# Kernel optimization log

Measured on AMD Instinct MI355X. Metric: run time of the kernel, lower is better.

Reference implementation:

```python
import jax, jax.numpy as jnp
import numpy as np

N, D, DFF, E, TOPK = 32768, 256, 1024, 8, 2


def setup_inputs() -> dict:
    key = jax.random.key(0)
    ks = jax.random.split(key, 5)
    return {
        "x": jax.random.normal(ks[0], (N, D), dtype=jnp.float32),
        "gate_w": jax.random.normal(ks[1], (D, E), dtype=jnp.float32) * 0.02,
        "gate_b": jnp.zeros((E,), jnp.float32),
        "w1": jax.random.normal(ks[2], (E, D, DFF), dtype=jnp.float32) * 0.02,
        "b1": jnp.zeros((E, DFF), jnp.float32),
        "w2": jax.random.normal(ks[3], (E, DFF, D), dtype=jnp.float32) * 0.02,
        "b2": jnp.zeros((E, D), jnp.float32),
        "top_k": TOPK,
    }


def reference(x, gate_w, gate_b, w1, b1, w2, b2, top_k):
    # Gating network: linear -> softmax -> top-k (returns topk_vals, topk_idx)
    logits = x @ gate_w + gate_b                       # [N, E]
    probs = jax.nn.softmax(logits, axis=-1)
    topk_vals, topk_idx = jax.lax.top_k(probs, top_k)  # [N, K], [N, K]

    # Naive full-batch expert evaluation (every expert runs on every token),
    # faithful to the original loop that applies the selected expert to all of x.
    h = jax.nn.relu(jnp.einsum('nd,edf->enf', x, w1) + b1[:, None, :])  # [E, N, DFF]
    y = jnp.einsum('enf,efd->end', h, w2) + b2[:, None, :]              # [E, N, D]

    # Per-token gather of the top-k experts' outputs, then weighted sum.
    y = jnp.transpose(y, (1, 0, 2))                                      # [N, E, D]
    sel = jnp.take_along_axis(y, topk_idx[:, :, None], axis=1)           # [N, K, D]
    return jnp.sum(sel * topk_vals[:, :, None], axis=1)                  # [N, D]
```

## Files before the change

### kernel.cpp

```cpp
#include <hip/hip_runtime.h>

#define N_TOK 32768
#define D 256
#define DFF 1024
#define NE 8
#define TB 64

typedef __attribute__((ext_vector_type(16))) float f32x16;
typedef __attribute__((ext_vector_type(8)))  short bf16x8;

#define BARRIER() do {                                        \
    asm volatile("s_waitcnt lgkmcnt(0)" ::: "memory");        \
    __builtin_amdgcn_s_barrier();                             \
    __builtin_amdgcn_sched_barrier(0);                        \
} while (0)

__device__ __forceinline__ unsigned short f2bf(float f) {
    union { float f; unsigned u; } v; v.f = f;
    unsigned r = v.u + 0x7FFFu + ((v.u >> 16) & 1u);
    return (unsigned short)(r >> 16);
}

__global__ __launch_bounds__(256) void wf_prep(
    const float* __restrict__ w1, const float* __restrict__ w2,
    short* __restrict__ w1f, short* __restrict__ w2f) {
    const int b = blockIdx.x;
    if (b < 1024) {
        const int gid  = b * 256 + threadIdx.x;
        const int lane = gid & 63;
        const int frag = gid >> 6;
        const int dblk = frag & 15;
        const int fblk = (frag >> 4) & 31;
        const int e    = frag >> 9;
        const int l31 = lane & 31, g = lane >> 5;

        const float* src = w1 + ((size_t)e * 256 + dblk * 16 + g * 8) * 1024
                              + fblk * 32 + l31;
        unsigned u[4];
#pragma unroll
        for (int jp = 0; jp < 4; ++jp) {
            float a = src[(size_t)(jp * 2)     * 1024];
            float c = src[(size_t)(jp * 2 + 1) * 1024];
            u[jp] = (unsigned)f2bf(a) | ((unsigned)f2bf(c) << 16);
        }
        *(uint4*)(w1f + (size_t)gid * 8) = make_uint4(u[0], u[1], u[2], u[3]);
    } else {
        const int gid  = (b - 1024) * 256 + threadIdx.x;
        const int lane = gid & 63;
        const int frag = gid >> 6;
        const int fblk = frag & 63;
        const int cblk = (frag >> 6) & 7;
        const int e    = frag >> 9;
        const int l31 = lane & 31, g = lane >> 5;

        const float* src = w2 + ((size_t)e * 1024 + fblk * 16 + g * 8) * 256
                              + cblk * 32 + l31;
        unsigned u[4];
#pragma unroll
        for (int jp = 0; jp < 4; ++jp) {
            float a = src[(size_t)(jp * 2)     * 256];
            float c = src[(size_t)(jp * 2 + 1) * 256];
            u[jp] = (unsigned)f2bf(a) | ((unsigned)f2bf(c) << 16);
        }
        *(uint4*)(w2f + (size_t)gid * 8) = make_uint4(u[0], u[1], u[2], u[3]);
    }
}

__global__ __launch_bounds__(256) void gate_all(
    const float* __restrict__ x, const float* __restrict__ gw,
    const float* __restrict__ gb,
    int* __restrict__ cnt, int* __restrict__ bidx, float* __restrict__ bp,
    int2* __restrict__ opos) {
    __shared__ float gws[2048];
    __shared__ int   se1[256], se2[256];
    __shared__ float sp1[256], sp2[256];
    __shared__ int   hist[NE], base_[NE];

    const int tid = threadIdx.x;
#pragma unroll
    for (int i = 0; i < 8; ++i) gws[tid + 256 * i] = gw[tid + 256 * i];
    if (tid < NE) hist[tid] = 0;
    __syncthreads();

    const int t = blockIdx.x * 256 + tid;
    const float* xr = x + (size_t)t * D;

    double acc[NE];
#pragma unroll
    for (int e = 0; e < NE; ++e) acc[e] = 0.0;

    for (int d0 = 0; d0 < 256; d0 += 4) {
        float4 xv = *(const float4*)(xr + d0);
        float xa[4] = {xv.x, xv.y, xv.z, xv.w};
#pragma unroll
        for (int j = 0; j < 4; ++j) {
            float4 ga  = *(const float4*)&gws[(d0 + j) * 8];
            float4 gbb = *(const float4*)&gws[(d0 + j) * 8 + 4];
            double xd = (double)xa[j];
            acc[0] += xd * (double)ga.x;  acc[1] += xd * (double)ga.y;
            acc[2] += xd * (double)ga.z;  acc[3] += xd * (double)ga.w;
            acc[4] += xd * (double)gbb.x; acc[5] += xd * (double)gbb.y;
            acc[6] += xd * (double)gbb.z; acc[7] += xd * (double)gbb.w;
        }
    }

    double l[NE];
#pragma unroll
    for (int e = 0; e < NE; ++e) l[e] = acc[e] + (double)gb[e];
    int e1 = 0;
#pragma unroll
    for (int e = 1; e < NE; ++e) if (l[e] > l[e1]) e1 = e;
    int e2 = (e1 == 0) ? 1 : 0;
#pragma unroll
    for (int e = 0; e < NE; ++e) if (e != e1 && l[e] > l[e2]) e2 = e;

    double s = 0.0;
#pragma unroll
    for (int e = 0; e < NE; ++e) s += exp(l[e] - l[e1]);
    se1[tid] = e1; se2[tid] = e2;
    sp1[tid] = (float)(1.0 / s);
    sp2[tid] = (float)(exp(l[e2] - l[e1]) / s);
    __syncthreads();

    const int pos1 = atomicAdd(&hist[se1[tid]], 1);
    const int pos2 = atomicAdd(&hist[se2[tid]], 1);
    __syncthreads();
    if (tid < NE) base_[tid] = atomicAdd(&cnt[tid], hist[tid]);
    __syncthreads();

    const int o1 = se1[tid] * N_TOK + base_[se1[tid]] + pos1;
    const int o2 = se2[tid] * N_TOK + base_[se2[tid]] + pos2;
    bidx[o1] = t;  bp[o1] = sp1[tid];
    bidx[o2] = t;  bp[o2] = sp2[tid];
    opos[t] = make_int2(o1, o2);
}

__global__ __launch_bounds__(512, 4) void expert_ffn(
    const float* __restrict__ x,
    const short* __restrict__ w1f,
    const short* __restrict__ w2f,
    const float* __restrict__ b1, const float* __restrict__ b2,
    const int* __restrict__ cnt, const int* __restrict__ bidx,
    const float* __restrict__ bp, float* __restrict__ out,
    float* __restrict__ yp, int staged) {
    const int e    = blockIdx.x & 7;
    const int tile = blockIdx.x >> 3;
    const int n_e  = cnt[e];
    const int row0 = tile * TB;
    if (row0 >= n_e) return;

    __shared__ short xs[16 * 64 * 16];
    __shared__ short hs[32 * 512];
    __shared__ int   tok_s[TB];
    __shared__ float p_s[TB];

    const int tid  = threadIdx.x;
    const int lane = tid & 63, wid = tid >> 6;
    const int l31  = lane & 31, g = lane >> 5;

    if (tid < TB) {
        int r = row0 + tid;
        tok_s[tid] = (r < n_e) ? bidx[e * N_TOK + r] : -1;
        p_s[tid]   = (r < n_e) ? bp[e * N_TOK + r] : 0.f;
    }
    BARRIER();

    {
        const int tok = tid >> 3;
        const int tk  = tok_s[tok];
        const float* xrow = x + (size_t)(tk < 0 ? 0 : tk) * D;
#pragma unroll
        for (int i = 0; i < 2; ++i) {
            const int dblk = (tid & 7) * 2 + i;
            unsigned u[8];
            if (tk >= 0) {
#pragma unroll
                for (int q = 0; q < 4; ++q) {
                    float4 v = *(const float4*)(xrow + dblk * 16 + q * 4);
                    u[q * 2 + 0] = (unsigned)f2bf(v.x) | ((unsigned)f2bf(v.y) << 16);
                    u[q * 2 + 1] = (unsigned)f2bf(v.z) | ((unsigned)f2bf(v.w) << 16);
                }
            } else {
#pragma unroll
                for (int q = 0; q < 8; ++q) u[q] = 0;
            }
            short* dp = &xs[dblk * 1024 + tok * 16];
            *(uint4*)(dp)     = make_uint4(u[0], u[1], u[2], u[3]);
            *(uint4*)(dp + 8) = make_uint4(u[4], u[5], u[6], u[7]);
        }
    }

    f32x16 acc[2];
#pragma unroll
    for (int a = 0; a < 2; ++a)
#pragma unroll
        for (int r = 0; r < 16; ++r) acc[a][r] = 0.f;

    const short* w1e = w1f + (size_t)e * (32 * 16 * 512);
    const short* w2e = w2f + (size_t)e * (8 * 64 * 512);
    const float* b1e = b1 + e * DFF;

    BARRIER();

    for (int fc = 0; fc < 4; ++fc) {
        f32x16 h0, h1;
#pragma unroll
        for (int r = 0; r < 16; ++r) { h0[r] = 0.f; h1[r] = 0.f; }

        const short* w1p = w1e + ((size_t)(fc * 8 + wid) * 16) * 512 + lane * 8;
        __builtin_amdgcn_s_setprio(1);
        {
            bf16x8 a0 = *(const bf16x8*)(w1p);
            bf16x8 x0 = *(const bf16x8*)&xs[l31 * 16 + g * 8];
            bf16x8 x1 = *(const bf16x8*)&xs[512 + l31 * 16 + g * 8];
#pragma unroll
            for (int db = 0; db < 16; ++db) {
                bf16x8 an, y0, y1;
                if (db < 15) {
                    an = *(const bf16x8*)(w1p + (db + 1) * 512);
                    y0 = *(const bf16x8*)&xs[(db + 1) * 1024 + l31 * 16 + g * 8];
                    y1 = *(const bf16x8*)&xs[(db + 1) * 1024 + 512 + l31 * 16 + g * 8];
                }
                h0 = __builtin_amdgcn_mfma_f32_32x32x16_bf16(a0, x0, h0, 0, 0, 0);
                h1 = __builtin_amdgcn_mfma_f32_32x32x16_bf16(a0, x1, h1, 0, 0, 0);
                if (db < 15) { a0 = an; x0 = y0; x1 = y1; }
            }
        }
        __builtin_amdgcn_s_setprio(0);

        BARRIER();

#pragma unroll
        for (int tp = 0; tp < 2; ++tp) {
            const f32x16& hh = tp ? h1 : h0;
#pragma unroll
            for (int m = 0; m < 4; ++m) {
                float4 bq = *(const float4*)(b1e + fc * 256 + wid * 32 + 8 * m + 4 * g);
                float v0 = fmaxf(hh[4 * m + 0] + bq.x, 0.f);
                float v1 = fmaxf(hh[4 * m + 1] + bq.y, 0.f);
                float v2 = fmaxf(hh[4 * m + 2] + bq.z, 0.f);
                float v3 = fmaxf(hh[4 * m + 3] + bq.w, 0.f);
                uint2 pk;
                pk.x = (unsigned)f2bf(v0) | ((unsigned)f2bf(v1) << 16);
                pk.y = (unsigned)f2bf(v2) | ((unsigned)f2bf(v3) << 16);
                const int fragid = (2 * wid + (m >> 1)) * 2 + tp;
                *(uint2*)&hs[fragid * 512 + ((m & 1) * 32 + l31) * 8 + 4 * g] = pk;
            }
        }

        const short* w2p = w2e + ((size_t)wid * 64 + fc * 16) * 512 + lane * 8;
        bf16x8 wcur = *(const bf16x8*)(w2p);

        BARRIER();

        __builtin_amdgcn_s_setprio(1);
        {
            bf16x8 ha0 = *(const bf16x8*)&hs[0 * 512 + lane * 8];
            bf16x8 ha1 = *(const bf16x8*)&hs[1 * 512 + lane * 8];
#pragma unroll
            for (int kt = 0; kt < 16; ++kt) {
                bf16x8 wn, hb0, hb1;
                if (kt < 15) {
                    wn  = *(const bf16x8*)(w2p + (kt + 1) * 512);
                    hb0 = *(const bf16x8*)&hs[((kt + 1) * 2 + 0) * 512 + lane * 8];
                    hb1 = *(const bf16x8*)&hs[((kt + 1) * 2 + 1) * 512 + lane * 8];
                }
                acc[0] = __builtin_amdgcn_mfma_f32_32x32x16_bf16(ha0, wcur, acc[0], 0, 0, 0);
                acc[1] = __builtin_amdgcn_mfma_f32_32x32x16_bf16(ha1, wcur, acc[1], 0, 0, 0);
                if (kt < 15) { wcur = wn; ha0 = hb0; ha1 = hb1; }
            }
        }
        __builtin_amdgcn_s_setprio(0);
    }

    const float* b2e = b2 + e * D;
    const int col = wid * 32 + l31;
    const float bv = b2e[col];
    if (staged) {
        float* ype = yp + ((size_t)e * N_TOK + row0) * 256;
#pragma unroll
        for (int tp = 0; tp < 2; ++tp) {
#pragma unroll
            for (int r = 0; r < 16; ++r) {
                const int tl = tp * 32 + (r & 3) + 8 * (r >> 2) + 4 * g;
                if (tok_s[tl] >= 0)
                    __builtin_nontemporal_store(
                        (acc[tp][r] + bv) * p_s[tl],
                        &ype[(size_t)tl * 256 + col]);
            }
        }
    } else {
#pragma unroll
        for (int tp = 0; tp < 2; ++tp) {
#pragma unroll
            for (int r = 0; r < 16; ++r) {
                const int tl = tp * 32 + (r & 3) + 8 * (r >> 2) + 4 * g;
                const int tk = tok_s[tl];
                if (tk >= 0)
                    atomicAdd(out + (size_t)tk * D + col,
                              (acc[tp][r] + bv) * p_s[tl]);
            }
        }
    }
}

__global__ __launch_bounds__(256) void combine(
    const float* __restrict__ yp, const int2* __restrict__ opos,
    float* __restrict__ out) {
    const int gid   = blockIdx.x * 256 + threadIdx.x;
    const int t     = gid >> 6;
    const int lane4 = gid & 63;
    const int2 o = opos[t];
    const float4 a = ((const float4*)yp)[(size_t)o.x * 64 + lane4];
    const float4 b = ((const float4*)yp)[(size_t)o.y * 64 + lane4];
    float4 r;
    r.x = a.x + b.x; r.y = a.y + b.y; r.z = a.z + b.z; r.w = a.w + b.w;
    ((float4*)out)[gid] = r;
}

extern "C" void kernel_launch(void* const* d_in, const int* in_sizes, int n_in,
                              void* d_out, int out_size, void* d_ws, size_t ws_size,
                              hipStream_t stream) {
    const float* x  = (const float*)d_in[0];
    const float* gw = (const float*)d_in[1];
    const float* gb = (const float*)d_in[2];
    const float* w1 = (const float*)d_in[3];
    const float* b1 = (const float*)d_in[4];
    const float* w2 = (const float*)d_in[5];
    const float* b2 = (const float*)d_in[6];
    float* out = (float*)d_out;

    char* ws = (char*)d_ws;
    size_t off = 0;
    int*   cnt   = (int*)(ws + off);  off += 256;
    int*   bidx  = (int*)(ws + off);  off += (size_t)NE * N_TOK * 4;
    float* bp    = (float*)(ws + off); off += (size_t)NE * N_TOK * 4;
    int2*  opos  = (int2*)(ws + off); off += (size_t)N_TOK * 8;
    short* w1f   = (short*)(ws + off); off += (size_t)NE * D * DFF * 2;
    short* w2f   = (short*)(ws + off); off += (size_t)NE * D * DFF * 2;
    float* yp    = (float*)(ws + off); off += (size_t)2 * N_TOK * D * 4;
    const int staged = (ws_size >= off) ? 1 : 0;

    hipMemsetAsync(cnt, 0, 256, stream);
    if (!staged)
        hipMemsetAsync(d_out, 0, (size_t)out_size * sizeof(float), stream);

    wf_prep<<<2048, 256, 0, stream>>>(w1, w2, w1f, w2f);
    gate_all<<<N_TOK / 256, 256, 0, stream>>>(x, gw, gb, cnt, bidx, bp, opos);
    expert_ffn<<<NE * (N_TOK / TB), 512, 0, stream>>>(x, w1f, w2f, b1, b2,
                                                      cnt, bidx, bp, out, yp, staged);
    if (staged)
        combine<<<(N_TOK * D / 4) / 256, 256, 0, stream>>>(yp, opos, out);
}
```

Measured before the change: 159.9 us.

## Merge weight prep with gating and deepen expert weight prefetch

```diff
diff --git a/kernel.cpp b/kernel.cpp
--- a/kernel.cpp
+++ b/kernel.cpp
@@ -21,56 +21,57 @@
     return (unsigned short)(r >> 16);
 }
 
-__global__ __launch_bounds__(256) void wf_prep(
+__global__ __launch_bounds__(256) void prep_gate(
     const float* __restrict__ w1, const float* __restrict__ w2,
-    short* __restrict__ w1f, short* __restrict__ w2f) {
-    const int b = blockIdx.x;
-    if (b < 1024) {
-        const int gid  = b * 256 + threadIdx.x;
-        const int lane = gid & 63;
-        const int frag = gid >> 6;
-        const int dblk = frag & 15;
-        const int fblk = (frag >> 4) & 31;
-        const int e    = frag >> 9;
-        const int l31 = lane & 31, g = lane >> 5;
-
-        const float* src = w1 + ((size_t)e * 256 + dblk * 16 + g * 8) * 1024
-                              + fblk * 32 + l31;
-        unsigned u[4];
-#pragma unroll
-        for (int jp = 0; jp < 4; ++jp) {
-            float a = src[(size_t)(jp * 2)     * 1024];
-            float c = src[(size_t)(jp * 2 + 1) * 1024];
-            u[jp] = (unsigned)f2bf(a) | ((unsigned)f2bf(c) << 16);
-        }
-        *(uint4*)(w1f + (size_t)gid * 8) = make_uint4(u[0], u[1], u[2], u[3]);
-    } else {
-        const int gid  = (b - 1024) * 256 + threadIdx.x;
-        const int lane = gid & 63;
-        const int frag = gid >> 6;
-        const int fblk = frag & 63;
-        const int cblk = (frag >> 6) & 7;
-        const int e    = frag >> 9;
-        const int l31 = lane & 31, g = lane >> 5;
-
-        const float* src = w2 + ((size_t)e * 1024 + fblk * 16 + g * 8) * 256
-                              + cblk * 32 + l31;
-        unsigned u[4];
-#pragma unroll
-        for (int jp = 0; jp < 4; ++jp) {
-            float a = src[(size_t)(jp * 2)     * 256];
-            float c = src[(size_t)(jp * 2 + 1) * 256];
-            u[jp] = (unsigned)f2bf(a) | ((unsigned)f2bf(c) << 16);
-        }
-        *(uint4*)(w2f + (size_t)gid * 8) = make_uint4(u[0], u[1], u[2], u[3]);
-    }
-}
-
-__global__ __launch_bounds__(256) void gate_all(
+    short* __restrict__ w1f, short* __restrict__ w2f,
     const float* __restrict__ x, const float* __restrict__ gw,
     const float* __restrict__ gb,
     int* __restrict__ cnt, int* __restrict__ bidx, float* __restrict__ bp,
     int2* __restrict__ opos) {
+    const int b = blockIdx.x;
+    if (b < 2048) {
+        if (b < 1024) {
+            const int gid  = b * 256 + threadIdx.x;
+            const int lane = gid & 63;
+            const int frag = gid >> 6;
+            const int dblk = frag & 15;
+            const int fblk = (frag >> 4) & 31;
+            const int e    = frag >> 9;
+            const int l31 = lane & 31, g = lane >> 5;
+
+            const float* src = w1 + ((size_t)e * 256 + dblk * 16 + g * 8) * 1024
+                                  + fblk * 32 + l31;
+            unsigned u[4];
+#pragma unroll
+            for (int jp = 0; jp < 4; ++jp) {
+                float a = src[(size_t)(jp * 2)     * 1024];
+                float c = src[(size_t)(jp * 2 + 1) * 1024];
+                u[jp] = (unsigned)f2bf(a) | ((unsigned)f2bf(c) << 16);
+            }
+            *(uint4*)(w1f + (size_t)gid * 8) = make_uint4(u[0], u[1], u[2], u[3]);
+        } else {
+            const int gid  = (b - 1024) * 256 + threadIdx.x;
+            const int lane = gid & 63;
+            const int frag = gid >> 6;
+            const int fblk = frag & 63;
+            const int cblk = (frag >> 6) & 7;
+            const int e    = frag >> 9;
+            const int l31 = lane & 31, g = lane >> 5;
+
+            const float* src = w2 + ((size_t)e * 1024 + fblk * 16 + g * 8) * 256
+                                  + cblk * 32 + l31;
+            unsigned u[4];
+#pragma unroll
+            for (int jp = 0; jp < 4; ++jp) {
+                float a = src[(size_t)(jp * 2)     * 256];
+                float c = src[(size_t)(jp * 2 + 1) * 256];
+                u[jp] = (unsigned)f2bf(a) | ((unsigned)f2bf(c) << 16);
+            }
+            *(uint4*)(w2f + (size_t)gid * 8) = make_uint4(u[0], u[1], u[2], u[3]);
+        }
+        return;
+    }
+
     __shared__ float gws[2048];
     __shared__ int   se1[256], se2[256];
     __shared__ float sp1[256], sp2[256];
@@ -82,7 +83,7 @@
     if (tid < NE) hist[tid] = 0;
     __syncthreads();
 
-    const int t = blockIdx.x * 256 + tid;
+    const int t = (b - 2048) * 256 + tid;
     const float* xr = x + (size_t)t * D;
 
     double acc[NE];
@@ -200,33 +201,47 @@
     const short* w2e = w2f + (size_t)e * (8 * 64 * 512);
     const float* b1e = b1 + e * DFF;
 
+    bf16x8 w1r[4];
+    {
+        const short* w1p0 = w1e + ((size_t)(0 * 8 + wid) * 16) * 512 + lane * 8;
+#pragma unroll
+        for (int k = 0; k < 4; ++k) w1r[k] = *(const bf16x8*)(w1p0 + k * 512);
+    }
+
     BARRIER();
 
     for (int fc = 0; fc < 4; ++fc) {
+        const short* w1p = w1e + ((size_t)(fc * 8 + wid) * 16) * 512 + lane * 8;
+
         f32x16 h0, h1;
 #pragma unroll
         for (int r = 0; r < 16; ++r) { h0[r] = 0.f; h1[r] = 0.f; }
 
-        const short* w1p = w1e + ((size_t)(fc * 8 + wid) * 16) * 512 + lane * 8;
         __builtin_amdgcn_s_setprio(1);
         {
-            bf16x8 a0 = *(const bf16x8*)(w1p);
             bf16x8 x0 = *(const bf16x8*)&xs[l31 * 16 + g * 8];
             bf16x8 x1 = *(const bf16x8*)&xs[512 + l31 * 16 + g * 8];
 #pragma unroll
             for (int db = 0; db < 16; ++db) {
-                bf16x8 an, y0, y1;
+                bf16x8 wa = w1r[db & 3];
+                if (db < 12)
+                    w1r[db & 3] = *(const bf16x8*)(w1p + (db + 4) * 512);
+                bf16x8 y0, y1;
                 if (db < 15) {
-                    an = *(const bf16x8*)(w1p + (db + 1) * 512);
                     y0 = *(const bf16x8*)&xs[(db + 1) * 1024 + l31 * 16 + g * 8];
                     y1 = *(const bf16x8*)&xs[(db + 1) * 1024 + 512 + l31 * 16 + g * 8];
                 }
-                h0 = __builtin_amdgcn_mfma_f32_32x32x16_bf16(a0, x0, h0, 0, 0, 0);
-                h1 = __builtin_amdgcn_mfma_f32_32x32x16_bf16(a0, x1, h1, 0, 0, 0);
-                if (db < 15) { a0 = an; x0 = y0; x1 = y1; }
+                h0 = __builtin_amdgcn_mfma_f32_32x32x16_bf16(wa, x0, h0, 0, 0, 0);
+                h1 = __builtin_amdgcn_mfma_f32_32x32x16_bf16(wa, x1, h1, 0, 0, 0);
+                if (db < 15) { x0 = y0; x1 = y1; }
             }
         }
         __builtin_amdgcn_s_setprio(0);
+
+        const short* w2p = w2e + ((size_t)wid * 64 + fc * 16) * 512 + lane * 8;
+        bf16x8 w2r[4];
+#pragma unroll
+        for (int k = 0; k < 4; ++k) w2r[k] = *(const bf16x8*)(w2p + k * 512);
 
         BARRIER();
 
@@ -248,10 +263,13 @@
             }
         }
 
-        const short* w2p = w2e + ((size_t)wid * 64 + fc * 16) * 512 + lane * 8;
-        bf16x8 wcur = *(const bf16x8*)(w2p);
-
         BARRIER();
+
+        if (fc < 3) {
+            const short* w1n = w1e + ((size_t)((fc + 1) * 8 + wid) * 16) * 512 + lane * 8;
+#pragma unroll
+            for (int k = 0; k < 4; ++k) w1r[k] = *(const bf16x8*)(w1n + k * 512);
+        }
 
         __builtin_amdgcn_s_setprio(1);
         {
@@ -259,15 +277,17 @@
             bf16x8 ha1 = *(const bf16x8*)&hs[1 * 512 + lane * 8];
 #pragma unroll
             for (int kt = 0; kt < 16; ++kt) {
-                bf16x8 wn, hb0, hb1;
+                bf16x8 wa = w2r[kt & 3];
+                if (kt < 12)
+                    w2r[kt & 3] = *(const bf16x8*)(w2p + (kt + 4) * 512);
+                bf16x8 hb0, hb1;
                 if (kt < 15) {
-                    wn  = *(const bf16x8*)(w2p + (kt + 1) * 512);
                     hb0 = *(const bf16x8*)&hs[((kt + 1) * 2 + 0) * 512 + lane * 8];
                     hb1 = *(const bf16x8*)&hs[((kt + 1) * 2 + 1) * 512 + lane * 8];
                 }
-                acc[0] = __builtin_amdgcn_mfma_f32_32x32x16_bf16(ha0, wcur, acc[0], 0, 0, 0);
-                acc[1] = __builtin_amdgcn_mfma_f32_32x32x16_bf16(ha1, wcur, acc[1], 0, 0, 0);
-                if (kt < 15) { wcur = wn; ha0 = hb0; ha1 = hb1; }
+                acc[0] = __builtin_amdgcn_mfma_f32_32x32x16_bf16(ha0, wa, acc[0], 0, 0, 0);
+                acc[1] = __builtin_amdgcn_mfma_f32_32x32x16_bf16(ha1, wa, acc[1], 0, 0, 0);
+                if (kt < 15) { ha0 = hb0; ha1 = hb1; }
             }
         }
         __builtin_amdgcn_s_setprio(0);
@@ -345,8 +365,8 @@
     if (!staged)
         hipMemsetAsync(d_out, 0, (size_t)out_size * sizeof(float), stream);
 
-    wf_prep<<<2048, 256, 0, stream>>>(w1, w2, w1f, w2f);
-    gate_all<<<N_TOK / 256, 256, 0, stream>>>(x, gw, gb, cnt, bidx, bp, opos);
+    prep_gate<<<2048 + N_TOK / 256, 256, 0, stream>>>(
+        w1, w2, w1f, w2f, x, gw, gb, cnt, bidx, bp, opos);
     expert_ffn<<<NE * (N_TOK / TB), 512, 0, stream>>>(x, w1f, w2f, b1, b2,
                                                       cnt, bidx, bp, out, yp, staged);
     if (staged)
```

New measurement: 162.0 us. Within noise of the previous version (+1.3%).

## Fuse weight prep, x bf16 conversion and gating into one kernel; compact staging buffer

Applied to the files above, without the earlier changes.

```diff
diff --git a/kernel.cpp b/kernel.cpp
--- a/kernel.cpp
+++ b/kernel.cpp
@@ -15,15 +15,19 @@
     __builtin_amdgcn_sched_barrier(0);                        \
 } while (0)
 
-__device__ __forceinline__ unsigned short f2bf(float f) {
-    union { float f; unsigned u; } v; v.f = f;
-    unsigned r = v.u + 0x7FFFu + ((v.u >> 16) & 1u);
-    return (unsigned short)(r >> 16);
-}
-
-__global__ __launch_bounds__(256) void wf_prep(
+__device__ __forceinline__ unsigned cvtpk(float lo, float hi) {
+    unsigned r;
+    asm("v_cvt_pk_bf16_f32 %0, %1, %2" : "=v"(r) : "v"(lo), "v"(hi));
+    return r;
+}
+
+__global__ __launch_bounds__(256) void prep_gate(
     const float* __restrict__ w1, const float* __restrict__ w2,
-    short* __restrict__ w1f, short* __restrict__ w2f) {
+    short* __restrict__ w1f, short* __restrict__ w2f,
+    const float* __restrict__ x, short* __restrict__ xb,
+    const float* __restrict__ gw, const float* __restrict__ gb,
+    int* __restrict__ cnt, int* __restrict__ bidx, float* __restrict__ bp,
+    int2* __restrict__ opos) {
     const int b = blockIdx.x;
     if (b < 1024) {
         const int gid  = b * 256 + threadIdx.x;
@@ -38,13 +42,13 @@
                               + fblk * 32 + l31;
         unsigned u[4];
 #pragma unroll
-        for (int jp = 0; jp < 4; ++jp) {
-            float a = src[(size_t)(jp * 2)     * 1024];
-            float c = src[(size_t)(jp * 2 + 1) * 1024];
-            u[jp] = (unsigned)f2bf(a) | ((unsigned)f2bf(c) << 16);
-        }
+        for (int jp = 0; jp < 4; ++jp)
+            u[jp] = cvtpk(src[(size_t)(jp * 2) * 1024],
+                          src[(size_t)(jp * 2 + 1) * 1024]);
         *(uint4*)(w1f + (size_t)gid * 8) = make_uint4(u[0], u[1], u[2], u[3]);
-    } else {
+        return;
+    }
+    if (b < 2048) {
         const int gid  = (b - 1024) * 256 + threadIdx.x;
         const int lane = gid & 63;
         const int frag = gid >> 6;
@@ -57,20 +61,24 @@
                               + cblk * 32 + l31;
         unsigned u[4];
 #pragma unroll
-        for (int jp = 0; jp < 4; ++jp) {
-            float a = src[(size_t)(jp * 2)     * 256];
-            float c = src[(size_t)(jp * 2 + 1) * 256];
-            u[jp] = (unsigned)f2bf(a) | ((unsigned)f2bf(c) << 16);
-        }
+        for (int jp = 0; jp < 4; ++jp)
+            u[jp] = cvtpk(src[(size_t)(jp * 2) * 256],
+                          src[(size_t)(jp * 2 + 1) * 256]);
         *(uint4*)(w2f + (size_t)gid * 8) = make_uint4(u[0], u[1], u[2], u[3]);
-    }
-}
-
-__global__ __launch_bounds__(256) void gate_all(
-    const float* __restrict__ x, const float* __restrict__ gw,
-    const float* __restrict__ gb,
-    int* __restrict__ cnt, int* __restrict__ bidx, float* __restrict__ bp,
-    int2* __restrict__ opos) {
+        return;
+    }
+    if (b < 6144) {
+        const int gid = (b - 2048) * 256 + threadIdx.x;
+        const float* s = x + (size_t)gid * 8;
+        float4 a = *(const float4*)(s);
+        float4 c = *(const float4*)(s + 4);
+        uint4 o;
+        o.x = cvtpk(a.x, a.y);  o.y = cvtpk(a.z, a.w);
+        o.z = cvtpk(c.x, c.y);  o.w = cvtpk(c.z, c.w);
+        *(uint4*)(xb + (size_t)gid * 8) = o;
+        return;
+    }
+
     __shared__ float gws[2048];
     __shared__ int   se1[256], se2[256];
     __shared__ float sp1[256], sp2[256];
@@ -82,7 +90,7 @@
     if (tid < NE) hist[tid] = 0;
     __syncthreads();
 
-    const int t = blockIdx.x * 256 + tid;
+    const int t = (b - 6144) * 256 + tid;
     const float* xr = x + (size_t)t * D;
 
     double acc[NE];
@@ -136,7 +144,7 @@
 }
 
 __global__ __launch_bounds__(512, 4) void expert_ffn(
-    const float* __restrict__ x,
+    const short* __restrict__ xb,
     const short* __restrict__ w1f,
     const short* __restrict__ w2f,
     const float* __restrict__ b1, const float* __restrict__ b2,
@@ -158,6 +166,9 @@
     const int lane = tid & 63, wid = tid >> 6;
     const int l31  = lane & 31, g = lane >> 5;
 
+    int cbase = 0;
+    for (int j = 0; j < e; ++j) cbase += cnt[j];
+
     if (tid < TB) {
         int r = row0 + tid;
         tok_s[tid] = (r < n_e) ? bidx[e * N_TOK + r] : -1;
@@ -168,25 +179,18 @@
     {
         const int tok = tid >> 3;
         const int tk  = tok_s[tok];
-        const float* xrow = x + (size_t)(tk < 0 ? 0 : tk) * D;
+        const short* xrow = xb + (size_t)(tk < 0 ? 0 : tk) * D;
 #pragma unroll
         for (int i = 0; i < 2; ++i) {
             const int dblk = (tid & 7) * 2 + i;
-            unsigned u[8];
+            uint4 v0 = make_uint4(0, 0, 0, 0), v1 = make_uint4(0, 0, 0, 0);
             if (tk >= 0) {
-#pragma unroll
-                for (int q = 0; q < 4; ++q) {
-                    float4 v = *(const float4*)(xrow + dblk * 16 + q * 4);
-                    u[q * 2 + 0] = (unsigned)f2bf(v.x) | ((unsigned)f2bf(v.y) << 16);
-                    u[q * 2 + 1] = (unsigned)f2bf(v.z) | ((unsigned)f2bf(v.w) << 16);
-                }
-            } else {
-#pragma unroll
-                for (int q = 0; q < 8; ++q) u[q] = 0;
+                v0 = *(const uint4*)(xrow + dblk * 16);
+                v1 = *(const uint4*)(xrow + dblk * 16 + 8);
             }
             short* dp = &xs[dblk * 1024 + tok * 16];
-            *(uint4*)(dp)     = make_uint4(u[0], u[1], u[2], u[3]);
-            *(uint4*)(dp + 8) = make_uint4(u[4], u[5], u[6], u[7]);
+            *(uint4*)(dp)     = v0;
+            *(uint4*)(dp + 8) = v1;
         }
     }
 
@@ -241,8 +245,8 @@
                 float v2 = fmaxf(hh[4 * m + 2] + bq.z, 0.f);
                 float v3 = fmaxf(hh[4 * m + 3] + bq.w, 0.f);
                 uint2 pk;
-                pk.x = (unsigned)f2bf(v0) | ((unsigned)f2bf(v1) << 16);
-                pk.y = (unsigned)f2bf(v2) | ((unsigned)f2bf(v3) << 16);
+                pk.x = cvtpk(v0, v1);
+                pk.y = cvtpk(v2, v3);
                 const int fragid = (2 * wid + (m >> 1)) * 2 + tp;
                 *(uint2*)&hs[fragid * 512 + ((m & 1) * 32 + l31) * 8 + 4 * g] = pk;
             }
@@ -277,7 +281,7 @@
     const int col = wid * 32 + l31;
     const float bv = b2e[col];
     if (staged) {
-        float* ype = yp + ((size_t)e * N_TOK + row0) * 256;
+        float* ype = yp + ((size_t)(cbase + row0)) * 256;
 #pragma unroll
         for (int tp = 0; tp < 2; ++tp) {
 #pragma unroll
@@ -306,13 +310,22 @@
 
 __global__ __launch_bounds__(256) void combine(
     const float* __restrict__ yp, const int2* __restrict__ opos,
-    float* __restrict__ out) {
+    const int* __restrict__ cnt, float* __restrict__ out) {
+    __shared__ int cb[NE];
+    if (threadIdx.x == 0) {
+        int s = 0;
+#pragma unroll
+        for (int j = 0; j < NE; ++j) { cb[j] = s; s += cnt[j]; }
+    }
+    __syncthreads();
     const int gid   = blockIdx.x * 256 + threadIdx.x;
     const int t     = gid >> 6;
     const int lane4 = gid & 63;
     const int2 o = opos[t];
-    const float4 a = ((const float4*)yp)[(size_t)o.x * 64 + lane4];
-    const float4 b = ((const float4*)yp)[(size_t)o.y * 64 + lane4];
+    const size_t r1 = (size_t)(cb[o.x >> 15] + (o.x & (N_TOK - 1)));
+    const size_t r2 = (size_t)(cb[o.y >> 15] + (o.y & (N_TOK - 1)));
+    const float4 a = ((const float4*)yp)[r1 * 64 + lane4];
+    const float4 b = ((const float4*)yp)[r2 * 64 + lane4];
     float4 r;
     r.x = a.x + b.x; r.y = a.y + b.y; r.z = a.z + b.z; r.w = a.w + b.w;
     ((float4*)out)[gid] = r;
@@ -338,6 +351,7 @@
     int2*  opos  = (int2*)(ws + off); off += (size_t)N_TOK * 8;
     short* w1f   = (short*)(ws + off); off += (size_t)NE * D * DFF * 2;
     short* w2f   = (short*)(ws + off); off += (size_t)NE * D * DFF * 2;
+    short* xb    = (short*)(ws + off); off += (size_t)N_TOK * D * 2;
     float* yp    = (float*)(ws + off); off += (size_t)2 * N_TOK * D * 4;
     const int staged = (ws_size >= off) ? 1 : 0;
 
@@ -345,10 +359,10 @@
     if (!staged)
         hipMemsetAsync(d_out, 0, (size_t)out_size * sizeof(float), stream);
 
-    wf_prep<<<2048, 256, 0, stream>>>(w1, w2, w1f, w2f);
-    gate_all<<<N_TOK / 256, 256, 0, stream>>>(x, gw, gb, cnt, bidx, bp, opos);
-    expert_ffn<<<NE * (N_TOK / TB), 512, 0, stream>>>(x, w1f, w2f, b1, b2,
+    prep_gate<<<2048 + 4096 + N_TOK / 256, 256, 0, stream>>>(
+        w1, w2, w1f, w2f, x, xb, gw, gb, cnt, bidx, bp, opos);
+    expert_ffn<<<NE * (N_TOK / TB), 512, 0, stream>>>(xb, w1f, w2f, b1, b2,
                                                       cnt, bidx, bp, out, yp, staged);
     if (staged)
-        combine<<<(N_TOK * D / 4) / 256, 256, 0, stream>>>(yp, opos, out);
-}
+        combine<<<(N_TOK * D / 4) / 256, 256, 0, stream>>>(yp, opos, cnt, out);
+}
```

Result: slower. 171.0 us (+7.0%).
